# Performance work log

Measured on AMD Instinct MI355X. Metric: run time of the kernel, lower is better.

Reference implementation:

```python
import jax, jax.numpy as jnp
import numpy as np

B, T, C = 2, 2048, 2048
H, HKV = 32, 8
D = C // H            # head_dim = 64
G = H // HKV          # groups = 4
ROPE_BASE = 10000.0


def _rotate_half(x):
    x1, x2 = jnp.split(x, 2, axis=-1)
    return jnp.concatenate((-x2, x1), axis=-1)


def _rope_tables(seq_len, dim):
    inv_freq = 1.0 / (ROPE_BASE ** (jnp.arange(0, dim, 2, dtype=jnp.float32) / dim))
    t = jnp.arange(seq_len, dtype=jnp.float32)
    freqs = jnp.outer(t, inv_freq)          # [T, D/2]
    emb = jnp.concatenate((freqs, freqs), axis=-1)  # [T, D]
    return jnp.cos(emb), jnp.sin(emb)


def setup_inputs() -> dict:
    key = jax.random.key(0)
    ks = jax.random.split(key, 5)
    s = 0.02
    return {
        "x": jax.random.normal(ks[0], (B, T, C), jnp.float32),
        "Wq": jax.random.normal(ks[1], (C, C), jnp.float32) * s,
        "Wk": jax.random.normal(ks[2], (HKV * D, C), jnp.float32) * s,
        "Wv": jax.random.normal(ks[3], (HKV * D, C), jnp.float32) * s,
        "Wo": jax.random.normal(ks[4], (C, C), jnp.float32) * s,
    }


def reference(x, Wq, Wk, Wv, Wo):
    b, t, c = x.shape
    # fused QKV projections (nn.Linear: y = x @ W.T)
    q = (x @ Wq.T).reshape(b, t, H, D).transpose(0, 2, 1, 3)      # [B,H,T,D]
    k = (x @ Wk.T).reshape(b, t, HKV, D).transpose(0, 2, 1, 3)    # [B,HKV,T,D]
    v = (x @ Wv.T).reshape(b, t, HKV, D).transpose(0, 2, 1, 3)

    # RoPE (start_pos = 0)
    cos, sin = _rope_tables(t, D)           # [T, D] each
    cos = cos[None, None]                   # [1,1,T,D]
    sin = sin[None, None]
    q = q * cos + _rotate_half(q) * sin
    k = k * cos + _rotate_half(k) * sin

    # GQA head expansion (repeat_interleave on head dim)
    k = jnp.repeat(k, G, axis=1)            # [B,H,T,D]
    v = jnp.repeat(v, G, axis=1)

    # causal attention
    scale = 1.0 / jnp.sqrt(jnp.asarray(D, jnp.float32))
    scores = jnp.einsum('bhqd,bhkd->bhqk', q, k) * scale          # [B,H,T,T]
    causal = jnp.tril(jnp.ones((t, t), dtype=bool))
    scores = jnp.where(causal[None, None], scores, -jnp.inf)
    attn = jax.nn.softmax(scores.astype(jnp.float32), axis=-1).astype(q.dtype)
    out = jnp.einsum('bhqk,bhkd->bhqd', attn, v)                  # [B,H,T,D]
    out = out.transpose(0, 2, 1, 3).reshape(b, t, c)
    return out @ Wo.T
```

## Files before the change

kernel.cpp:

```cpp
#include <hip/hip_runtime.h>
#include <hip/hip_bf16.h>
#include <math.h>

typedef short short8 __attribute__((ext_vector_type(8)));
typedef float floatx4 __attribute__((ext_vector_type(4)));

typedef __attribute__((address_space(1))) unsigned int as1_u32;
typedef __attribute__((address_space(3))) unsigned int as3_u32;

__device__ __forceinline__ void load_lds16(const void* g, void* l) {
  __builtin_amdgcn_global_load_lds((const as1_u32*)g, (as3_u32*)l, 16, 0, 0);
}

__device__ __forceinline__ unsigned short f2bf(float f) {
  __bf16 h = (__bf16)f;
  return __builtin_bit_cast(unsigned short, h);
}

#define TB 2
#define TT 2048
#define TC 2048
#define QKN 2560
#define KOFF 2048
#define SCALE_Q 0.18033688f

__global__ __launch_bounds__(256) void cast_all(
    const float* __restrict__ x, const float* __restrict__ wq,
    const float* __restrict__ wk, const float* __restrict__ wv,
    const float* __restrict__ wo,
    unsigned short* __restrict__ xb, unsigned short* __restrict__ wqkv,
    unsigned short* __restrict__ wob, float2* __restrict__ ropeTab) {
  if (blockIdx.x < 256) {
    const int idx = blockIdx.x * 256 + threadIdx.x;
    const int t = idx >> 5, d = idx & 31;
    const float inv = exp2f((float)d * -0.4152410119f);
    float sn, cs;
    sincosf((float)t * inv, &sn, &cs);
    ropeTab[idx] = make_float2(cs, sn);
  }
  long i4 = (long)blockIdx.x * 256 + threadIdx.x;
  const float* src;
  unsigned short* dst;
  if (i4 < 2097152)      { src = x;  dst = xb; }
  else if (i4 < 3145728) { src = wq; dst = wqkv;           i4 -= 2097152; }
  else if (i4 < 3407872) { src = wk; dst = wqkv + 4194304; i4 -= 3145728; }
  else if (i4 < 3670016) { src = wv; dst = wqkv + 5242880; i4 -= 3407872; }
  else                   { src = wo; dst = wob;            i4 -= 3670016; }
  float4 v = ((const float4*)src)[i4];
  ushort4 o;
  o.x = f2bf(v.x); o.y = f2bf(v.y); o.z = f2bf(v.z); o.w = f2bf(v.w);
  ((ushort4*)dst)[i4] = o;
}

__global__ __launch_bounds__(256) void gemm_qkv(const unsigned short* __restrict__ A,
                                                const unsigned short* __restrict__ Bw,
                                                unsigned short* __restrict__ qk,
                                                unsigned short* __restrict__ vT,
                                                const float2* __restrict__ ropeTab) {
  __shared__ unsigned short As[128 * 64];
  __shared__ unsigned short Bs[128 * 64];
  const int K = 2048;
  const int tid = threadIdx.x;
  const int lane = tid & 63, w = tid >> 6;
  const int quad = lane >> 4, l15 = lane & 15;
  const int wm = w >> 1, wn = w & 1;
  const int lin = blockIdx.y * 24 + blockIdx.x;
  const int sub = lin >> 3;
  const int m0 = (sub / 3) * 128;
  const int n0 = ((lin & 7) * 3 + sub % 3) * 128;

  floatx4 acc[4][4];
#pragma unroll
  for (int i = 0; i < 4; ++i)
#pragma unroll
    for (int j = 0; j < 4; ++j) acc[i][j] = (floatx4){0.f, 0.f, 0.f, 0.f};

  const int ar = tid >> 3;
  const int ac = (((tid & 7) ^ (ar & 7)) * 8);
  const unsigned short* Abase = A + (size_t)(m0 + ar) * K + ac;
  const unsigned short* Bbase = Bw + (size_t)(n0 + ar) * K + ac;

  for (int k0 = 0; k0 < K; k0 += 64) {
    __syncthreads();
#pragma unroll
    for (int p = 0; p < 4; ++p) {
      load_lds16(Abase + (size_t)(p * 32) * K + k0, (char*)As + p * 4096 + tid * 16);
      load_lds16(Bbase + (size_t)(p * 32) * K + k0, (char*)Bs + p * 4096 + tid * 16);
    }
    __syncthreads();
#pragma unroll
    for (int ks = 0; ks < 2; ++ks) {
      short8 af[4], bfr[4];
      const int key = (((ks << 2) + quad) ^ (l15 & 7)) << 4;
#pragma unroll
      for (int i = 0; i < 4; ++i)
        af[i] = *(const short8*)((const char*)As + (wm * 64 + i * 16 + l15) * 128 + key);
#pragma unroll
      for (int j = 0; j < 4; ++j)
        bfr[j] = *(const short8*)((const char*)Bs + (wn * 64 + j * 16 + l15) * 128 + key);
#pragma unroll
      for (int i = 0; i < 4; ++i)
#pragma unroll
        for (int j = 0; j < 4; ++j)
          acc[i][j] = __builtin_amdgcn_mfma_f32_16x16x32_bf16(af[i], bfr[j], acc[i][j], 0, 0, 0);
    }
  }

  const int colb = n0 + wn * 64;
  if (colb < QKN) {
    const float qscale = (colb < KOFF) ? SCALE_Q : 1.0f;
#pragma unroll
    for (int i = 0; i < 4; ++i) {
      const int rowb = m0 + wm * 64 + i * 16 + quad * 4;
      const int tb = rowb & (TT - 1);
#pragma unroll
      for (int j = 0; j < 2; ++j) {
        const int col = colb + j * 16 + l15;
        const int d = j * 16 + l15;
#pragma unroll
        for (int r = 0; r < 4; ++r) {
          const float2 cssn = ropeTab[(tb + r) * 32 + d];
          const float a = acc[i][j][r], b2 = acc[i][j + 2][r];
          const float qa = (a * cssn.x - b2 * cssn.y) * qscale;
          const float qb = (b2 * cssn.x + a * cssn.y) * qscale;
          unsigned short* p = qk + (size_t)(rowb + r) * QKN + col;
          p[0] = f2bf(qa);
          p[32] = f2bf(qb);
        }
      }
    }
  } else {
#pragma unroll
    for (int i = 0; i < 4; ++i) {
      const int rowb = m0 + wm * 64 + i * 16 + quad * 4;
#pragma unroll
      for (int j = 0; j < 4; ++j) {
        const int col = colb + j * 16 + l15;
        ushort4 pk;
        pk.x = f2bf(acc[i][j][0]); pk.y = f2bf(acc[i][j][1]);
        pk.z = f2bf(acc[i][j][2]); pk.w = f2bf(acc[i][j][3]);
        *(ushort4*)(vT + (size_t)(col - 2560) * 4096 + rowb) = pk;
      }
    }
  }
}

__global__ __launch_bounds__(256) void gemm_nt_f32(const unsigned short* __restrict__ A,
                                                   const unsigned short* __restrict__ Bw,
                                                   float* __restrict__ C,
                                                   int M, int N, int K) {
  __shared__ unsigned short As[128 * 64];
  __shared__ unsigned short Bs[128 * 64];
  const int tid = threadIdx.x;
  const int lane = tid & 63, w = tid >> 6;
  const int quad = lane >> 4, l15 = lane & 15;
  const int wm = w >> 1, wn = w & 1;
  const int lin = blockIdx.y * 16 + blockIdx.x;
  const int sub = lin >> 3;
  const int m0 = (sub >> 1) * 128;
  const int n0 = ((lin & 7) * 2 + (sub & 1)) * 128;

  floatx4 acc[4][4];
#pragma unroll
  for (int i = 0; i < 4; ++i)
#pragma unroll
    for (int j = 0; j < 4; ++j) acc[i][j] = (floatx4){0.f, 0.f, 0.f, 0.f};

  const int ar = tid >> 3;
  const int ac = (((tid & 7) ^ (ar & 7)) * 8);
  const unsigned short* Abase = A + (size_t)(m0 + ar) * K + ac;
  const unsigned short* Bbase = Bw + (size_t)(n0 + ar) * K + ac;

  for (int k0 = 0; k0 < K; k0 += 64) {
    __syncthreads();
#pragma unroll
    for (int p = 0; p < 4; ++p) {
      load_lds16(Abase + (size_t)(p * 32) * K + k0, (char*)As + p * 4096 + tid * 16);
      load_lds16(Bbase + (size_t)(p * 32) * K + k0, (char*)Bs + p * 4096 + tid * 16);
    }
    __syncthreads();
#pragma unroll
    for (int ks = 0; ks < 2; ++ks) {
      short8 af[4], bfr[4];
      const int key = (((ks << 2) + quad) ^ (l15 & 7)) << 4;
#pragma unroll
      for (int i = 0; i < 4; ++i)
        af[i] = *(const short8*)((const char*)As + (wm * 64 + i * 16 + l15) * 128 + key);
#pragma unroll
      for (int j = 0; j < 4; ++j)
        bfr[j] = *(const short8*)((const char*)Bs + (wn * 64 + j * 16 + l15) * 128 + key);
#pragma unroll
      for (int i = 0; i < 4; ++i)
#pragma unroll
        for (int j = 0; j < 4; ++j)
          acc[i][j] = __builtin_amdgcn_mfma_f32_16x16x32_bf16(af[i], bfr[j], acc[i][j], 0, 0, 0);
    }
  }
#pragma unroll
  for (int i = 0; i < 4; ++i) {
    const int row = m0 + wm * 64 + i * 16 + quad * 4;
#pragma unroll
    for (int j = 0; j < 4; ++j) {
      const int col = n0 + wn * 64 + j * 16 + l15;
#pragma unroll
      for (int r = 0; r < 4; ++r)
        C[(size_t)(row + r) * N + col] = acc[i][j][r];
    }
  }
}

__global__ __launch_bounds__(256) void attn_kernel(const unsigned short* __restrict__ qk,
                                                   const unsigned short* __restrict__ vT,
                                                   unsigned short* __restrict__ attn) {
  const int h = blockIdx.x, b = blockIdx.y;
  const int qt = 15 - (int)blockIdx.z;
  const int hk = h >> 2;
  const int tid = threadIdx.x;
  const int w = tid >> 6, lane = tid & 63, quad = lane >> 4, l15 = lane & 15;

  __shared__ char lds[51200];
  unsigned short* Pq = (unsigned short*)(lds + 32768 + w * 4608);

  const int srow = tid >> 3;
  const int sgrp = ((tid & 7) ^ (srow & 7));
  const int relbase = w * 32 + l15;

  const short8 ones = {16256, 16256, 16256, 16256, 16256, 16256, 16256, 16256};

  const size_t rowQ = (size_t)(b * TT + qt * 128);

  {
    const unsigned short* qsrc = qk + (rowQ + srow) * QKN + h * 64 + sgrp * 8;
#pragma unroll
    for (int p = 0; p < 4; ++p)
      load_lds16(qsrc + (size_t)p * 32 * QKN, lds + p * 4096 + tid * 16);
  }
  __syncthreads();
  short8 qf[2][2];
#pragma unroll
  for (int i = 0; i < 2; ++i)
#pragma unroll
    for (int ks = 0; ks < 2; ++ks)
      qf[i][ks] = *(const short8*)(lds + (w * 32 + i * 16 + l15) * 128 +
                                   ((((ks << 2) + quad) ^ (l15 & 7)) << 4));
  __syncthreads();

  floatx4 accO[2][4], accL[2];
#pragma unroll
  for (int i = 0; i < 2; ++i) {
    accL[i] = (floatx4){0.f, 0.f, 0.f, 0.f};
#pragma unroll
    for (int j = 0; j < 4; ++j) accO[i][j] = (floatx4){0.f, 0.f, 0.f, 0.f};
  }

  const unsigned short* kptr =
      qk + (size_t)(b * TT + srow) * QKN + KOFF + hk * 64 + sgrp * 8;
  const unsigned short* vptr =
      vT + (size_t)(hk * 64 + srow) * 4096 + b * TT + sgrp * 8;

  load_lds16(kptr, lds + tid * 16);
  load_lds16(kptr + (size_t)32 * QKN, lds + 4096 + tid * 16);
  load_lds16(vptr, lds + 16384 + tid * 16);
  load_lds16(vptr + (size_t)32 * 4096, lds + 16384 + 4096 + tid * 16);
  kptr += (size_t)64 * QKN;
  vptr += 64;
  __syncthreads();

  auto step = [&](const int BUF, const bool PREF, const int MREL) {
    if (PREF) {
      char* kd = lds + ((BUF ^ 1) * 8192);
      char* vd = lds + 16384 + ((BUF ^ 1) * 8192);
      load_lds16(kptr, kd + tid * 16);
      load_lds16(kptr + (size_t)32 * QKN, kd + 4096 + tid * 16);
      load_lds16(vptr, vd + tid * 16);
      load_lds16(vptr + (size_t)32 * 4096, vd + 4096 + tid * 16);
      kptr += (size_t)64 * QKN;
      vptr += 64;
    }

    const char* Ks = lds + BUF * 8192;
    floatx4 st[2][4];
    __builtin_amdgcn_s_setprio(1);
#pragma unroll
    for (int jm = 0; jm < 4; ++jm) {
      const int krow = jm * 16 + l15;
      const short8 kf0 = *(const short8*)(Ks + krow * 128 + ((quad ^ (l15 & 7)) << 4));
      const short8 kf1 = *(const short8*)(Ks + krow * 128 + (((4 + quad) ^ (l15 & 7)) << 4));
#pragma unroll
      for (int i = 0; i < 2; ++i) {
        floatx4 z = (floatx4){0.f, 0.f, 0.f, 0.f};
        z = __builtin_amdgcn_mfma_f32_16x16x32_bf16(kf0, qf[i][0], z, 0, 0, 0);
        st[i][jm] = __builtin_amdgcn_mfma_f32_16x16x32_bf16(kf1, qf[i][1], z, 0, 0, 0);
      }
    }
    __builtin_amdgcn_s_setprio(0);

    const char* Vt = lds + 16384 + BUF * 8192;
    short8 vf[2][4];
#pragma unroll
    for (int ks = 0; ks < 2; ++ks)
#pragma unroll
      for (int jd = 0; jd < 4; ++jd) {
        const int d = jd * 16 + l15;
        vf[ks][jd] = *(const short8*)(Vt + d * 128 +
                                      ((((ks << 2) + quad) ^ (l15 & 7)) << 4));
      }

#pragma unroll
    for (int i = 0; i < 2; ++i) {
#pragma unroll
      for (int jm = 0; jm < 4; ++jm) {
        float e0 = exp2f(st[i][jm][0]);
        float e1 = exp2f(st[i][jm][1]);
        float e2 = exp2f(st[i][jm][2]);
        float e3 = exp2f(st[i][jm][3]);
        if (MREL >= 0) {
          const int rel = relbase + i * 16 - MREL;
          const int kg = jm * 16 + quad * 4;
          if (kg > rel) e0 = 0.f;
          if (kg + 1 > rel) e1 = 0.f;
          if (kg + 2 > rel) e2 = 0.f;
          if (kg + 3 > rel) e3 = 0.f;
        }
        ushort4 pk;
        pk.x = f2bf(e0); pk.y = f2bf(e1); pk.z = f2bf(e2); pk.w = f2bf(e3);
        *(ushort4*)(Pq + (i * 16 + l15) * 72 + jm * 16 + quad * 4) = pk;
      }
    }
    asm volatile("s_waitcnt lgkmcnt(0)" ::: "memory");

    __builtin_amdgcn_s_setprio(1);
#pragma unroll
    for (int ks = 0; ks < 2; ++ks) {
      short8 pf[2];
#pragma unroll
      for (int i2 = 0; i2 < 2; ++i2)
        pf[i2] = *(const short8*)(Pq + (i2 * 16 + l15) * 72 + ks * 32 + quad * 8);
      accL[0] = __builtin_amdgcn_mfma_f32_16x16x32_bf16(pf[0], ones, accL[0], 0, 0, 0);
      accL[1] = __builtin_amdgcn_mfma_f32_16x16x32_bf16(pf[1], ones, accL[1], 0, 0, 0);
#pragma unroll
      for (int jd = 0; jd < 4; ++jd) {
        accO[0][jd] = __builtin_amdgcn_mfma_f32_16x16x32_bf16(pf[0], vf[ks][jd], accO[0][jd], 0, 0, 0);
        accO[1][jd] = __builtin_amdgcn_mfma_f32_16x16x32_bf16(pf[1], vf[ks][jd], accO[1][jd], 0, 0, 0);
      }
    }
    __builtin_amdgcn_s_setprio(0);
    __syncthreads();
  };

  for (int t2 = 0; t2 < qt; ++t2) {
    step(0, true, -1);
    step(1, true, -1);
  }
  step(0, true, 0);
  step(1, false, 64);

#pragma unroll
  for (int i2 = 0; i2 < 2; ++i2) {
#pragma unroll
    for (int jd = 0; jd < 4; ++jd) {
      const int col = h * 64 + jd * 16 + l15;
#pragma unroll
      for (int r = 0; r < 4; ++r) {
        const size_t row = rowQ + w * 32 + i2 * 16 + quad * 4 + r;
        attn[row * TC + col] = f2bf(accO[i2][jd][r] / accL[i2][r]);
      }
    }
  }
}

extern "C" void kernel_launch(void* const* d_in, const int* in_sizes, int n_in,
                              void* d_out, int out_size, void* d_ws, size_t ws_size,
                              hipStream_t stream) {
  const float* x = (const float*)d_in[0];
  const float* Wq = (const float*)d_in[1];
  const float* Wk = (const float*)d_in[2];
  const float* Wv = (const float*)d_in[3];
  const float* Wo = (const float*)d_in[4];
  float* out = (float*)d_out;

  char* ws = (char*)d_ws;
  unsigned short* xb   = (unsigned short*)(ws);
  unsigned short* wqkv = (unsigned short*)(ws + 16777216);
  unsigned short* wob  = (unsigned short*)(ws + 29360128);
  unsigned short* qk   = (unsigned short*)(ws + 37748736);
  unsigned short* vT   = (unsigned short*)(ws + 58720256);
  unsigned short* attn = (unsigned short*)(ws + 62914560);
  float2* ropeTab = (float2*)(ws + 62914560);

  cast_all<<<18432, 256, 0, stream>>>(x, Wq, Wk, Wv, Wo, xb, wqkv, wob, ropeTab);
  gemm_qkv<<<dim3(24, 32), 256, 0, stream>>>(xb, wqkv, qk, vT, ropeTab);
  attn_kernel<<<dim3(32, 2, 16), 256, 0, stream>>>(qk, vT, attn);
  gemm_nt_f32<<<dim3(16, 32), 256, 0, stream>>>(attn, wob, out, 4096, TC, 2048);
}
```

Measured before the change: 292.4 us.

## Transpose attention probabilities in registers with permlane swaps instead of LDS

Replaces the per-wave LDS round trip that turned the score-layout probabilities into MFMA A-operand layout with gfx950 permlane32/permlane16 swap instructions done in registers. This removes the P scratch region, shrinking shared memory from 51200 to 32768 bytes, and the launch bounds now ask for 4 blocks per CU so occupancy can rise. The risk is register pressure under the tighter bound and getting the lane-permutation mapping right.

```diff
diff --git a/kernel.cpp b/kernel.cpp
--- a/kernel.cpp
+++ b/kernel.cpp
@@ -4,6 +4,8 @@
 
 typedef short short8 __attribute__((ext_vector_type(8)));
 typedef float floatx4 __attribute__((ext_vector_type(4)));
+typedef unsigned int uintx4 __attribute__((ext_vector_type(4)));
+typedef int intx2 __attribute__((ext_vector_type(2)));
 
 typedef __attribute__((address_space(1))) unsigned int as1_u32;
 typedef __attribute__((address_space(3))) unsigned int as3_u32;
@@ -15,6 +17,10 @@
 __device__ __forceinline__ unsigned short f2bf(float f) {
   __bf16 h = (__bf16)f;
   return __builtin_bit_cast(unsigned short, h);
+}
+
+__device__ __forceinline__ unsigned int pack_bf16(float a, float b) {
+  return (unsigned int)f2bf(a) | ((unsigned int)f2bf(b) << 16);
 }
 
 #define TB 2
@@ -209,17 +215,16 @@
   }
 }
 
-__global__ __launch_bounds__(256) void attn_kernel(const unsigned short* __restrict__ qk,
-                                                   const unsigned short* __restrict__ vT,
-                                                   unsigned short* __restrict__ attn) {
+__global__ __launch_bounds__(256, 4) void attn_kernel(const unsigned short* __restrict__ qk,
+                                                      const unsigned short* __restrict__ vT,
+                                                      unsigned short* __restrict__ attn) {
   const int h = blockIdx.x, b = blockIdx.y;
   const int qt = 15 - (int)blockIdx.z;
   const int hk = h >> 2;
   const int tid = threadIdx.x;
   const int w = tid >> 6, lane = tid & 63, quad = lane >> 4, l15 = lane & 15;
 
-  __shared__ char lds[51200];
-  unsigned short* Pq = (unsigned short*)(lds + 32768 + w * 4608);
+  __shared__ char lds[32768];
 
   const int srow = tid >> 3;
   const int sgrp = ((tid & 7) ^ (srow & 7));
@@ -306,8 +311,10 @@
                                       ((((ks << 2) + quad) ^ (l15 & 7)) << 4));
       }
 
+    short8 pT[2][2];
 #pragma unroll
     for (int i = 0; i < 2; ++i) {
+      unsigned int U[4][2];
 #pragma unroll
       for (int jm = 0; jm < 4; ++jm) {
         float e0 = exp2f(st[i][jm][0]);
@@ -322,26 +329,33 @@
           if (kg + 2 > rel) e2 = 0.f;
           if (kg + 3 > rel) e3 = 0.f;
         }
-        ushort4 pk;
-        pk.x = f2bf(e0); pk.y = f2bf(e1); pk.z = f2bf(e2); pk.w = f2bf(e3);
-        *(ushort4*)(Pq + (i * 16 + l15) * 72 + jm * 16 + quad * 4) = pk;
-      }
-    }
-    asm volatile("s_waitcnt lgkmcnt(0)" ::: "memory");
+        U[jm][0] = pack_bf16(e0, e1);
+        U[jm][1] = pack_bf16(e2, e3);
+      }
+#pragma unroll
+      for (int ks = 0; ks < 2; ++ks) {
+        uintx4 t;
+#pragma unroll
+        for (int hh = 0; hh < 2; ++hh) {
+          intx2 r32 = __builtin_amdgcn_permlane32_swap(
+              (int)U[2 * ks][hh], (int)U[2 * ks + 1][hh], false, false);
+          intx2 r16 = __builtin_amdgcn_permlane16_swap(r32[0], r32[1], false, false);
+          t[hh] = (unsigned int)r16[0];
+          t[2 + hh] = (unsigned int)r16[1];
+        }
+        pT[i][ks] = __builtin_bit_cast(short8, t);
+      }
+    }
 
     __builtin_amdgcn_s_setprio(1);
 #pragma unroll
     for (int ks = 0; ks < 2; ++ks) {
-      short8 pf[2];
-#pragma unroll
-      for (int i2 = 0; i2 < 2; ++i2)
-        pf[i2] = *(const short8*)(Pq + (i2 * 16 + l15) * 72 + ks * 32 + quad * 8);
-      accL[0] = __builtin_amdgcn_mfma_f32_16x16x32_bf16(pf[0], ones, accL[0], 0, 0, 0);
-      accL[1] = __builtin_amdgcn_mfma_f32_16x16x32_bf16(pf[1], ones, accL[1], 0, 0, 0);
+      accL[0] = __builtin_amdgcn_mfma_f32_16x16x32_bf16(pT[0][ks], ones, accL[0], 0, 0, 0);
+      accL[1] = __builtin_amdgcn_mfma_f32_16x16x32_bf16(pT[1][ks], ones, accL[1], 0, 0, 0);
 #pragma unroll
       for (int jd = 0; jd < 4; ++jd) {
-        accO[0][jd] = __builtin_amdgcn_mfma_f32_16x16x32_bf16(pf[0], vf[ks][jd], accO[0][jd], 0, 0, 0);
-        accO[1][jd] = __builtin_amdgcn_mfma_f32_16x16x32_bf16(pf[1], vf[ks][jd], accO[1][jd], 0, 0, 0);
+        accO[0][jd] = __builtin_amdgcn_mfma_f32_16x16x32_bf16(pT[0][ks], vf[ks][jd], accO[0][jd], 0, 0, 0);
+        accO[1][jd] = __builtin_amdgcn_mfma_f32_16x16x32_bf16(pT[1][ks], vf[ks][jd], accO[1][jd], 0, 0, 0);
       }
     }
     __builtin_amdgcn_s_setprio(0);
```

Measured after the change: 336.4 us. +15.0%, slower.
